# Optimization experiments

Hardware: AMD Instinct MI355X
Metric: run time of the kernel (lower is better)

The kernel has to match this reference:

```python
import jax, jax.numpy as jnp
import numpy as np

FS = 16000
M = 800            # win_length = 0.05*fs
K = 1024           # n_fft = next pow2
HOP = 600          # M - V, V = M//4
NBINS = 256        # 4000*K//fs
L_MAX = 13         # round(0.5*fs/hop)
L_MIN = 3
MIN_DB = 10.0
DEFAULT_RT60 = 0.5
EPS = 1e-10
INVALID = 1e30


def _stft_power(y):
    # y: [B,1,T] -> power spectrogram [B,1,NBINS,nF] (torchaudio Spectrogram, power=2,
    # center=True reflect pad, periodic hann of length M zero-padded centered to K)
    n = jnp.arange(M, dtype=y.dtype)
    win = 0.5 - 0.5 * jnp.cos(2.0 * jnp.pi * n / M)
    w = jnp.zeros(K, dtype=y.dtype).at[(K - M) // 2:(K - M) // 2 + M].set(win)
    yp = jnp.pad(y, ((0, 0), (0, 0), (K // 2, K // 2)), mode='reflect')
    nF = 1 + (yp.shape[-1] - K) // HOP
    idx = jnp.arange(nF)[:, None] * HOP + jnp.arange(K)[None, :]
    frames = yp[..., idx] * w                       # [B,1,nF,K]
    spec = jnp.abs(jnp.fft.rfft(frames)) ** 2       # [B,1,nF,K//2+1]
    return jnp.swapaxes(spec, -1, -2)[..., :NBINS, :]


def reference(y, coeffs):
    Y = _stft_power(y)                              # [B,1,F,T]
    B = Y.shape[0]
    T = Y.shape[-1]
    Yf = Y.reshape(B, -1, T)                        # [B,F,T] (mono channel folded)

    # --- strictly-decreasing run detection for every window length L in [3,13] ---
    d = (jnp.diff(Yf, axis=-1) < 0).astype(jnp.int32)                      # [B,F,T-1]
    c = jnp.concatenate([jnp.zeros_like(d[..., :1]), jnp.cumsum(d, -1)], -1)  # [B,F,T]
    Ls = jnp.arange(L_MIN, L_MAX + 1)               # [11]
    t = jnp.arange(T)
    end = jnp.minimum(t[None, :] + Ls[:, None] - 1, T - 1)                 # [11,T]
    cnt = jnp.take(c, end, axis=-1) - c[:, :, None, :]                     # [B,F,11,T]
    valid_t = (t[None, :] + Ls[:, None]) <= T                              # [11,T]
    dec = (cnt == (Ls - 1)[None, None, :, None]) & valid_t[None, None]     # [B,F,11,T]

    # per subband: largest L with any decreasing window (compute_individual_masks)
    hasL = dec.any(-1)                              # [B,F,11]
    chosen = (Ls.shape[0] - 1) - jnp.argmax(hasL[..., ::-1], -1)           # [B,F]
    has_any = hasL.any(-1)                          # [B,F]
    start_mask = jnp.take_along_axis(dec, chosen[..., None, None], axis=2)[:, :, 0, :]
    start_mask = start_mask & has_any[..., None]    # [B,F,T]
    lenL = L_MIN + chosen                           # [B,F] window length per subband

    # --- padded windows of length L_MAX for every start position ---
    widx = jnp.clip(t[:, None] + jnp.arange(L_MAX)[None, :], 0, T - 1)     # [T,13]
    W = jnp.take(Yf, widx, axis=-1)                 # [B,F,T,13]
    lm = (jnp.arange(L_MAX) < lenL[..., None])[:, :, None, :]              # [B,F,1,13]
    lmf = lm.astype(W.dtype)

    # EDC = reversed cumsum of power, in dB, rescaled to start at 0
    wm = W * lmf
    edc = jnp.cumsum(wm[..., ::-1], -1)[..., ::-1]
    edc_db = 10.0 * jnp.log10(jnp.maximum(edc, EPS))
    scaled = edc_db - edc_db[..., :1]               # [B,F,T,13]

    last_idx = jnp.broadcast_to((lenL - 1)[:, :, None, None], scaled.shape[:-1] + (1,))
    last = jnp.take_along_axis(scaled, last_idx, -1)[..., 0]               # [B,F,T]
    selected = last < -MIN_DB

    x = jnp.arange(L_MAX, dtype=scaled.dtype)
    nl = lenL.astype(scaled.dtype)[..., None]       # [B,F,1]
    xm = jnp.sum(x * lmf[:, :, 0, :], -1, keepdims=True) / nl              # [B,F,1]
    ym = jnp.sum(scaled * lmf, -1) / nl             # [B,F,T]
    xc = (x - xm[..., None]) * lmf                  # [B,F,1,13]
    num = jnp.sum(xc * (scaled - ym[..., None]), -1)                        # [B,F,T]
    den = jnp.sum(xc * xc, -1)                      # [B,F,1]
    slope = num / den

    valid = start_mask & selected
    slope_safe = jnp.where(valid, slope, -1.0)
    rt60 = (-60.0 / slope_safe) * (HOP / FS)        # [B,F,T]

    # per-batch lower median over all valid segments (torch.median semantics)
    vals = jnp.where(valid, rt60, INVALID).reshape(B, -1)
    nvalid = valid.reshape(B, -1).sum(-1)
    srt = jnp.sort(vals, -1)
    midx = jnp.maximum((nvalid - 1) // 2, 0)
    med = jnp.take_along_axis(srt, midx[:, None], -1)[:, 0]
    med = jnp.where(nvalid > 0, med, 0.0)

    corr = coeffs[0] + coeffs[1] * med              # degree-1 polynomial correction
    out = jnp.where(nvalid > 0, corr, DEFAULT_RT60)
    out = jnp.maximum(out, 0.01)
    return out[:, None, None]                       # [B,1,1]


def setup_inputs() -> dict:
    key = jax.random.key(0)
    k1, _ = jax.random.split(key)
    y = jax.random.normal(k1, (32, 1, 160000), dtype=jnp.float32)
    coeffs = jnp.array([0.0, 1.0], dtype=jnp.float32)  # identity polynomial init
    return {"y": y, "coeffs": coeffs}
```

## Files before the change

### kernel.cpp

```cpp
#include <hip/hip_runtime.h>
#include <hip/hip_bf16.h>
#include <math.h>

#define NB 32
#define TLEN 160000
#define HOP 600
#define NBINS 256
#define TT 267
#define TTP 268
#define NROWS (NB * NBINS)
#define LMAX 13

__device__ __forceinline__ unsigned f2key(float f) {
    unsigned b = __float_as_uint(f);
    return (b & 0x80000000u) ? ~b : (b | 0x80000000u);
}
__device__ __forceinline__ int P(int i) { return i + (i >> 4); }
__device__ __forceinline__ int Q(int i) { return i ^ ((i >> 4) & 0x3C); }
__device__ __forceinline__ float2 cmul(float2 a, float2 w) {
    return make_float2(a.x * w.x - a.y * w.y, a.x * w.y + a.y * w.x);
}
__device__ __forceinline__ float2 cadd(float2 a, float2 b) { return make_float2(a.x + b.x, a.y + b.y); }
__device__ __forceinline__ float2 csub(float2 a, float2 b) { return make_float2(a.x - b.x, a.y - b.y); }

__global__ void init_kernel(float2* __restrict__ tw, float* __restrict__ wtab) {
    int j = blockIdx.x * blockDim.x + threadIdx.x;
    if (j < 512) {
        double ang = -2.0 * 3.14159265358979323846 * (double)j / 1024.0;
        tw[j] = make_float2((float)cos(ang), (float)sin(ang));
    }
    if (j < 800) {
        float arg = (6.2831855f * (float)j) / 800.0f;
        wtab[j] = 0.5f - 0.5f * cosf(arg);
    }
}

__global__ __launch_bounds__(256) void stft_power_kernel(
        const float* __restrict__ y, const float2* __restrict__ twg,
        const float* __restrict__ wtab, float* __restrict__ Y) {
    __shared__ float2 zz[4][1024];
    __shared__ float2 twl[544];

    const int g = blockIdx.x;
    const int b = blockIdx.y;
    const int tid = threadIdx.x;
    const int f0 = 8 * g;

    for (int j = tid; j < 512; j += 256) twl[P(j)] = twg[j];

    const float* yb = y + (size_t)b * TLEN;
    #pragma unroll
    for (int a = 0; a < 4; ++a) {
        const int fa = f0 + 2 * a;
        if (fa >= TT) break;
        const bool hasB = (fa + 1 < TT);
        const int base = fa * HOP - 512;
        const int i = 4 * tid;
        float2 q4[4];
        if (base >= 0 && hasB) {
            if (i >= 112 && i < 912) {
                float4 w4 = *(const float4*)(wtab + (i - 112));
                float4 a0 = *(const float4*)(yb + base + i);
                float4 a1 = *(const float4*)(yb + base + HOP + i);
                q4[0] = make_float2(a0.x * w4.x, a1.x * w4.x);
                q4[1] = make_float2(a0.y * w4.y, a1.y * w4.y);
                q4[2] = make_float2(a0.z * w4.z, a1.z * w4.z);
                q4[3] = make_float2(a0.w * w4.w, a1.w * w4.w);
            } else {
                q4[0] = q4[1] = q4[2] = q4[3] = make_float2(0.f, 0.f);
            }
        } else {
            #pragma unroll
            for (int m = 0; m < 4; ++m) {
                const int ii = i + m;
                float v0 = 0.f, v1 = 0.f;
                if (ii >= 112 && ii < 912) {
                    float w = wtab[ii - 112];
                    int p0 = base + ii;
                    int q0 = p0 < 0 ? -p0 : p0;
                    v0 = yb[q0] * w;
                    if (hasB) v1 = yb[p0 + HOP] * w;
                }
                q4[m] = make_float2(v0, v1);
            }
        }
        float4* dst = (float4*)&zz[a][Q(i)];
        dst[0] = make_float4(q4[0].x, q4[0].y, q4[1].x, q4[1].y);
        dst[1] = make_float4(q4[2].x, q4[2].y, q4[3].x, q4[3].y);
    }
    __syncthreads();

    {
        const int a = tid >> 6, j = tid & 63;
        float2 x[16];
        #pragma unroll
        for (int k = 0; k < 16; ++k) x[k] = zz[a][Q(j + 64 * k)];
        #pragma unroll
        for (int k = 0; k < 8; ++k) {
            float2 s = csub(x[k], x[k + 8]);
            x[k] = cadd(x[k], x[k + 8]);
            x[k + 8] = cmul(s, twl[P(j + 64 * k)]);
        }
        #pragma unroll
        for (int h = 0; h < 16; h += 8)
            #pragma unroll
            for (int k = 0; k < 4; ++k) {
                float2 s = csub(x[h + k], x[h + k + 4]);
                x[h + k] = cadd(x[h + k], x[h + k + 4]);
                x[h + k + 4] = cmul(s, twl[P(2 * j + 128 * k)]);
            }
        #pragma unroll
        for (int h = 0; h < 16; h += 4)
            #pragma unroll
            for (int k = 0; k < 2; ++k) {
                float2 s = csub(x[h + k], x[h + k + 2]);
                x[h + k] = cadd(x[h + k], x[h + k + 2]);
                x[h + k + 2] = cmul(s, twl[P(4 * j + 256 * k)]);
            }
        {
            const float2 wD = twl[P(8 * j)];
            #pragma unroll
            for (int h = 0; h < 16; h += 2) {
                float2 s = csub(x[h], x[h + 1]);
                x[h] = cadd(x[h], x[h + 1]);
                x[h + 1] = cmul(s, wD);
            }
        }
        #pragma unroll
        for (int k = 0; k < 16; ++k) zz[a][Q(j + 64 * k)] = x[k];
    }
    __syncthreads();

    {
        const int a = tid >> 6, l = tid & 63;
        const int gg = l >> 2, j2 = l & 3;
        const int b0 = 64 * gg + j2;
        float2 x[16];
        #pragma unroll
        for (int k = 0; k < 16; ++k) x[k] = zz[a][Q(b0 + 4 * k)];
        #pragma unroll
        for (int k = 0; k < 8; ++k) {
            float2 s = csub(x[k], x[k + 8]);
            x[k] = cadd(x[k], x[k + 8]);
            x[k + 8] = cmul(s, twl[P(16 * j2 + 64 * k)]);
        }
        #pragma unroll
        for (int h = 0; h < 16; h += 8)
            #pragma unroll
            for (int k = 0; k < 4; ++k) {
                float2 s = csub(x[h + k], x[h + k + 4]);
                x[h + k] = cadd(x[h + k], x[h + k + 4]);
                x[h + k + 4] = cmul(s, twl[P(32 * j2 + 128 * k)]);
            }
        #pragma unroll
        for (int h = 0; h < 16; h += 4)
            #pragma unroll
            for (int k = 0; k < 2; ++k) {
                float2 s = csub(x[h + k], x[h + k + 2]);
                x[h + k] = cadd(x[h + k], x[h + k + 2]);
                x[h + k + 2] = cmul(s, twl[P(64 * (j2 + 4 * k))]);
            }
        {
            const float2 wD = twl[P(128 * j2)];
            #pragma unroll
            for (int h = 0; h < 16; h += 2) {
                float2 s = csub(x[h], x[h + 1]);
                x[h] = cadd(x[h], x[h + 1]);
                x[h + 1] = cmul(s, wD);
            }
        }
        #pragma unroll
        for (int k = 0; k < 16; ++k) zz[a][Q(b0 + 4 * k)] = x[k];
    }
    __syncthreads();

    #pragma unroll
    for (int a = 0; a < 4; ++a) {
        float4* pp = (float4*)&zz[a][Q(4 * tid)];
        float4 r0 = pp[0], r1 = pp[1];
        float2 x0 = make_float2(r0.x, r0.y), x1 = make_float2(r0.z, r0.w);
        float2 x2 = make_float2(r1.x, r1.y), x3 = make_float2(r1.z, r1.w);
        float2 e0 = cadd(x0, x2);
        float2 e1 = cadd(x1, x3);
        float2 d0 = csub(x0, x2);
        float2 d1 = csub(x1, x3);
        float2 d1m = make_float2(d1.y, -d1.x);
        pp[0] = make_float4(e0.x + e1.x, e0.y + e1.y, e0.x - e1.x, e0.y - e1.y);
        pp[1] = make_float4(d0.x + d1m.x, d0.y + d1m.y, d0.x - d1m.x, d0.y - d1m.y);
    }
    __syncthreads();

    const int k = tid;
    const int nk = (1024 - k) & 1023;
    const int rk = (int)(__brev((unsigned)k) >> 22);
    const int rn = (int)(__brev((unsigned)nk) >> 22);
    float* yrow = Y + ((size_t)b * NBINS + k) * TTP;
    if (g < 33) {
        float p[8];
        #pragma unroll
        for (int a = 0; a < 4; ++a) {
            float2 zk = zz[a][Q(rk)], zn = zz[a][Q(rn)];
            float x0r = 0.5f * (zk.x + zn.x), x0i = 0.5f * (zk.y - zn.y);
            float x1r = 0.5f * (zk.y + zn.y), x1i = 0.5f * (zn.x - zk.x);
            p[2 * a]     = x0r * x0r + x0i * x0i;
            p[2 * a + 1] = x1r * x1r + x1i * x1i;
        }
        *(float4*)(yrow + f0)     = make_float4(p[0], p[1], p[2], p[3]);
        *(float4*)(yrow + f0 + 4) = make_float4(p[4], p[5], p[6], p[7]);
    } else {
        #pragma unroll
        for (int a = 0; a < 4; ++a) {
            const int fb2 = f0 + 2 * a;
            if (fb2 >= TT) break;
            float2 zk = zz[a][Q(rk)], zn = zz[a][Q(rn)];
            float x0r = 0.5f * (zk.x + zn.x), x0i = 0.5f * (zk.y - zn.y);
            float x1r = 0.5f * (zk.y + zn.y), x1i = 0.5f * (zn.x - zk.x);
            if (fb2 + 1 < TT)
                *(float2*)(yrow + fb2) = make_float2(x0r * x0r + x0i * x0i,
                                                     x1r * x1r + x1i * x1i);
            else
                yrow[fb2] = x0r * x0r + x0i * x0i;
        }
    }
}

__global__ __launch_bounds__(256) void subband_kernel(
        const float* __restrict__ Y, unsigned* __restrict__ compact,
        int* __restrict__ rowcnt) {
    __shared__ float ys[4][272];

    const int tid = threadIdx.x;
    const int lane = tid & 63;
    const int wave = tid >> 6;
    const int row = blockIdx.x * 4 + wave;
    const float* src = Y + (size_t)row * TTP;

    float v[5];
    #pragma unroll
    for (int c = 0; c < 5; ++c) {
        int t = c * 64 + lane;
        v[c] = (t < TT) ? src[t] : 0.0f;
        if (t < TT) ys[wave][t] = v[c];
    }
    __syncthreads();

    const float* yy = ys[wave];

    unsigned long long m[5];
    #pragma unroll
    for (int c = 0; c < 5; ++c) {
        int t = c * 64 + lane;
        bool d = (t < TT - 1) && (yy[t + 1] < v[c]);
        m[c] = __ballot(d);
    }

    auto runl = [&](int c, int l) -> int {
        unsigned long long lo = m[c] >> l;
        if (l && c < 4) lo |= m[c + 1] << (64 - l);
        unsigned win = (unsigned)lo & 0xFFFu;
        return (win == 0xFFFu) ? 12 : (__ffs((int)~win) - 1);
    };

    int rl[5];
    int mx = 0;
    #pragma unroll
    for (int c = 0; c < 5; ++c) { rl[c] = runl(c, lane); mx = max(mx, rl[c]); }
    #pragma unroll
    for (int o = 32; o; o >>= 1) mx = max(mx, __shfl_xor(mx, o));
    const int maxrun = mx;

    if (maxrun < 2) {
        if (lane == 0) rowcnt[row] = 0;
        return;
    }
    const int L = maxrun + 1;

    float sumx = 0.0f;
    #pragma unroll
    for (int j = 0; j < LMAX; ++j) if (j < L) sumx += (float)j;
    const float xm = sumx / (float)L;
    float den = 0.0f;
    #pragma unroll
    for (int j = 0; j < LMAX; ++j) if (j < L) { float xc = (float)j - xm; den += xc * xc; }

    unsigned keys[5];
    unsigned long long vm[5];
    #pragma unroll
    for (int c = 0; c < 5; ++c) {
        const int t = c * 64 + lane;
        bool sel = false;
        unsigned key = 0u;
        if (rl[c] >= L - 1) {
            float edc[LMAX];
            float s = 0.0f;
            #pragma unroll
            for (int j = LMAX - 1; j >= 0; --j) {
                if (j < L) s += yy[t + j];
                edc[j] = s;
            }
            float db0 = 10.0f * log10f(fmaxf(edc[0], 1e-10f));
            float scl[LMAX];
            float s1 = 0.0f;
            float last = 0.0f;
            #pragma unroll
            for (int j = 0; j < LMAX; ++j) {
                if (j < L) {
                    float db = 10.0f * log10f(fmaxf(edc[j], 1e-10f));
                    float sc = db - db0;
                    scl[j] = sc;
                    s1 += sc;
                    if (j == L - 1) last = sc;
                }
            }
            if (last < -10.0f) {
                const float ym = s1 / (float)L;
                float num = 0.0f;
                #pragma unroll
                for (int j = 0; j < LMAX; ++j)
                    if (j < L) num += ((float)j - xm) * (scl[j] - ym);
                const float slope = num / den;
                float rt60 = (-60.0f / slope) * 0.0375f;
                sel = true;
                key = f2key(rt60);
            }
        }
        vm[c] = __ballot(sel);
        keys[c] = key;
    }

    unsigned* dst = compact + (size_t)row * TTP;
    const unsigned long long below = (1ull << lane) - 1ull;
    int base = 0;
    #pragma unroll
    for (int c = 0; c < 5; ++c) {
        if (vm[c] & (1ull << lane))
            dst[base + (int)__popcll(vm[c] & below)] = keys[c];
        base += (int)__popcll(vm[c]);
    }
    if (lane == 0) rowcnt[row] = base;
}

__global__ __launch_bounds__(256) void median_kernel(
        const unsigned* __restrict__ compact, const int* __restrict__ rowcnt,
        const float* __restrict__ coeffs, float* __restrict__ out) {
    __shared__ unsigned hist[16384];
    __shared__ unsigned wsum[4];
    __shared__ int sh_sel;
    __shared__ unsigned sh_kkc;
    __shared__ unsigned sh_kk, sh_prefix, sh_pmask;
    __shared__ int sh_n;

    const int b = blockIdx.x;
    const int tid = threadIdx.x;
    const int lane = tid & 63;
    const int wave = tid >> 6;
    const int myrow = b * NBINS + tid;
    const int myc = rowcnt[myrow];
    const unsigned* mykeys = compact + (size_t)myrow * TTP;

    {
        unsigned x = (unsigned)myc;
        #pragma unroll
        for (int o = 1; o < 64; o <<= 1) { unsigned t = __shfl_up(x, o); if (lane >= o) x += t; }
        if (lane == 63) wsum[wave] = x;
        __syncthreads();
        if (tid == 0) {
            int n = (int)(wsum[0] + wsum[1] + wsum[2] + wsum[3]);
            sh_n = n;
            sh_kk = (n > 0) ? (unsigned)((n - 1) / 2) : 0u;
            sh_prefix = 0u; sh_pmask = 0u;
        }
        __syncthreads();
    }
    const int n = sh_n;
    if (n == 0) {
        if (tid == 0) out[b] = 0.5f;
        return;
    }

    const int shifts[3] = {18, 4, 0};
    for (int p = 0; p < 3; ++p) {
        const int shift = shifts[p];
        const bool big = (p < 2);

        if (big) {
            uint4* h4 = (uint4*)hist;
            for (int i = tid; i < 4096; i += 256) h4[i] = make_uint4(0u, 0u, 0u, 0u);
        } else if (tid < 16) hist[tid] = 0u;
        __syncthreads();

        const unsigned pfx = sh_prefix, pm = sh_pmask;
        const unsigned bmask = big ? 16383u : 15u;
        for (int i = 0; i < myc; ++i) {
            unsigned k = mykeys[i];
            if ((k & pm) == pfx) atomicAdd(&hist[(k >> shift) & bmask], 1u);
        }
        __syncthreads();

        const unsigned kk = sh_kk;
        if (big) {
            unsigned s = 0;
            const int base = tid * 64;
            #pragma unroll 8
            for (int ii = 0; ii < 64; ++ii) s += hist[base + ((ii + tid) & 63)];
            unsigned x = s;
            #pragma unroll
            for (int o = 1; o < 64; o <<= 1) { unsigned t = __shfl_up(x, o); if (lane >= o) x += t; }
            if (lane == 63) wsum[wave] = x;
            __syncthreads();
            unsigned woff = 0;
            for (int w = 0; w < wave; ++w) woff += wsum[w];
            const unsigned incl = x + woff, excl = incl - s;
            if (kk >= excl && kk < incl) { sh_sel = tid; sh_kkc = kk - excl; }
            __syncthreads();
            const int sel = sh_sel;
            const unsigned kkc = sh_kkc;
            if (wave == 0) {
                unsigned h = hist[sel * 64 + lane];
                unsigned xx = h;
                #pragma unroll
                for (int o = 1; o < 64; o <<= 1) { unsigned t = __shfl_up(xx, o); if (lane >= o) xx += t; }
                unsigned ex = xx - h;
                if (kkc >= ex && kkc < xx) {
                    sh_prefix = pfx | ((unsigned)(sel * 64 + lane) << shift);
                    sh_pmask  = pm | (16383u << shift);
                    sh_kk = kkc - ex;
                }
            }
            __syncthreads();
        } else {
            if (wave == 0) {
                unsigned h = (lane < 16) ? hist[lane] : 0u;
                unsigned xx = h;
                #pragma unroll
                for (int o = 1; o < 64; o <<= 1) { unsigned t = __shfl_up(xx, o); if (lane >= o) xx += t; }
                unsigned ex = xx - h;
                if (lane < 16 && kk >= ex && kk < xx)
                    sh_prefix = pfx | (unsigned)lane;
            }
            __syncthreads();
        }
    }

    if (tid == 0) {
        unsigned kx = sh_prefix;
        unsigned fb = (kx & 0x80000000u) ? (kx & 0x7FFFFFFFu) : ~kx;
        float med = __uint_as_float(fb);
        out[b] = fmaxf(coeffs[0] + coeffs[1] * med, 0.01f);
    }
}

extern "C" void kernel_launch(void* const* d_in, const int* in_sizes, int n_in,
                              void* d_out, int out_size, void* d_ws, size_t ws_size,
                              hipStream_t stream) {
    const float* y = (const float*)d_in[0];
    const float* coeffs = (const float*)d_in[1];
    float* out = (float*)d_out;

    const size_t YB = (size_t)NROWS * TTP * sizeof(float);
    char* base = (char*)d_ws;
    float* Y = (float*)base;
    unsigned* compact = (unsigned*)(base + YB);
    int* rowcnt = (int*)(base + 2 * YB);
    float2* tw = (float2*)(base + 2 * YB + (size_t)NROWS * sizeof(int));
    float* wtab = (float*)((char*)tw + 512 * sizeof(float2));

    init_kernel<<<4, 256, 0, stream>>>(tw, wtab);
    stft_power_kernel<<<dim3((TT + 7) / 8, NB), 256, 0, stream>>>(y, tw, wtab, Y);
    subband_kernel<<<NROWS / 4, 256, 0, stream>>>(Y, compact, rowcnt);
    median_kernel<<<NB, 256, 0, stream>>>(compact, rowcnt, coeffs, out);
}
```

Measured before the change: 104.6 us.

## Stage median keys in LDS and use 12/12/8-bit radix select passes

The median kernel now compacts each batch's valid keys into shared memory once, using a prefix-sum offset per row. Each radix pass then scans those keys with all threads striding over them, instead of every thread re-reading its own row from global memory with uneven per-thread counts. The radix digits change from 14/14/4 bits to 12/12/8, which shrinks the histogram to 4096 bins so it is cheaper to clear and scan. This costs extra LDS (64KB of key staging) and keeps a global-memory fallback for when there are more than 16384 keys.

```diff
diff --git a/kernel.cpp b/kernel.cpp
--- a/kernel.cpp
+++ b/kernel.cpp
@@ -343,12 +343,11 @@
 __global__ __launch_bounds__(256) void median_kernel(
         const unsigned* __restrict__ compact, const int* __restrict__ rowcnt,
         const float* __restrict__ coeffs, float* __restrict__ out) {
-    __shared__ unsigned hist[16384];
+    __shared__ unsigned lkeys[16384];
+    __shared__ unsigned hist[4096];
     __shared__ unsigned wsum[4];
-    __shared__ int sh_sel;
-    __shared__ unsigned sh_kkc;
-    __shared__ unsigned sh_kk, sh_prefix, sh_pmask;
-    __shared__ int sh_n;
+    __shared__ unsigned sh_kk, sh_kkc, sh_prefix, sh_pmask;
+    __shared__ int sh_sel, sh_n;
 
     const int b = blockIdx.x;
     const int tid = threadIdx.x;
@@ -358,85 +357,95 @@
     const int myc = rowcnt[myrow];
     const unsigned* mykeys = compact + (size_t)myrow * TTP;
 
-    {
-        unsigned x = (unsigned)myc;
-        #pragma unroll
-        for (int o = 1; o < 64; o <<= 1) { unsigned t = __shfl_up(x, o); if (lane >= o) x += t; }
-        if (lane == 63) wsum[wave] = x;
-        __syncthreads();
-        if (tid == 0) {
-            int n = (int)(wsum[0] + wsum[1] + wsum[2] + wsum[3]);
-            sh_n = n;
-            sh_kk = (n > 0) ? (unsigned)((n - 1) / 2) : 0u;
-            sh_prefix = 0u; sh_pmask = 0u;
-        }
-        __syncthreads();
-    }
+    unsigned x = (unsigned)myc;
+    #pragma unroll
+    for (int o = 1; o < 64; o <<= 1) { unsigned t = __shfl_up(x, o); if (lane >= o) x += t; }
+    if (lane == 63) wsum[wave] = x;
+    __syncthreads();
+    unsigned woff = 0;
+    for (int w = 0; w < wave; ++w) woff += wsum[w];
+    const int myoff = (int)(woff + x) - myc;
+    if (tid == 0) {
+        int n = (int)(wsum[0] + wsum[1] + wsum[2] + wsum[3]);
+        sh_n = n;
+        sh_kk = (n > 0) ? (unsigned)((n - 1) / 2) : 0u;
+        sh_prefix = 0u; sh_pmask = 0u;
+    }
+    __syncthreads();
     const int n = sh_n;
     if (n == 0) {
         if (tid == 0) out[b] = 0.5f;
         return;
     }
 
-    const int shifts[3] = {18, 4, 0};
+    const bool inlds = (n <= 16384);
+    if (inlds)
+        for (int i = 0; i < myc; ++i) lkeys[myoff + i] = mykeys[i];
+    __syncthreads();
+
+    const int shifts[3] = {20, 8, 0};
     for (int p = 0; p < 3; ++p) {
         const int shift = shifts[p];
         const bool big = (p < 2);
-
+        const unsigned bmask = big ? 4095u : 255u;
+
+        {
+            uint4* h4 = (uint4*)hist;
+            for (int i = tid; i < 1024; i += 256) h4[i] = make_uint4(0u, 0u, 0u, 0u);
+        }
+        __syncthreads();
+
+        const unsigned pfx = sh_prefix, pm = sh_pmask;
+        if (inlds) {
+            for (int i = tid; i < n; i += 256) {
+                unsigned k = lkeys[i];
+                if ((k & pm) == pfx) atomicAdd(&hist[(k >> shift) & bmask], 1u);
+            }
+        } else {
+            for (int i = 0; i < myc; ++i) {
+                unsigned k = mykeys[i];
+                if ((k & pm) == pfx) atomicAdd(&hist[(k >> shift) & bmask], 1u);
+            }
+        }
+        __syncthreads();
+
+        const unsigned kk = sh_kk;
+        unsigned s = 0;
         if (big) {
-            uint4* h4 = (uint4*)hist;
-            for (int i = tid; i < 4096; i += 256) h4[i] = make_uint4(0u, 0u, 0u, 0u);
-        } else if (tid < 16) hist[tid] = 0u;
+            const int base2 = tid * 16;
+            #pragma unroll
+            for (int ii = 0; ii < 16; ++ii) s += hist[base2 + ((ii + tid) & 15)];
+        } else {
+            s = hist[tid];
+        }
+        unsigned xs = s;
+        #pragma unroll
+        for (int o = 1; o < 64; o <<= 1) { unsigned t = __shfl_up(xs, o); if (lane >= o) xs += t; }
+        if (lane == 63) wsum[wave] = xs;
         __syncthreads();
-
-        const unsigned pfx = sh_prefix, pm = sh_pmask;
-        const unsigned bmask = big ? 16383u : 15u;
-        for (int i = 0; i < myc; ++i) {
-            unsigned k = mykeys[i];
-            if ((k & pm) == pfx) atomicAdd(&hist[(k >> shift) & bmask], 1u);
+        unsigned wo = 0;
+        for (int w = 0; w < wave; ++w) wo += wsum[w];
+        const unsigned incl = xs + wo, excl = incl - s;
+        if (kk >= excl && kk < incl) {
+            if (big) { sh_sel = tid; sh_kkc = kk - excl; }
+            else     { sh_prefix = pfx | (unsigned)tid; }
         }
         __syncthreads();
 
-        const unsigned kk = sh_kk;
         if (big) {
-            unsigned s = 0;
-            const int base = tid * 64;
-            #pragma unroll 8
-            for (int ii = 0; ii < 64; ++ii) s += hist[base + ((ii + tid) & 63)];
-            unsigned x = s;
-            #pragma unroll
-            for (int o = 1; o < 64; o <<= 1) { unsigned t = __shfl_up(x, o); if (lane >= o) x += t; }
-            if (lane == 63) wsum[wave] = x;
-            __syncthreads();
-            unsigned woff = 0;
-            for (int w = 0; w < wave; ++w) woff += wsum[w];
-            const unsigned incl = x + woff, excl = incl - s;
-            if (kk >= excl && kk < incl) { sh_sel = tid; sh_kkc = kk - excl; }
-            __syncthreads();
             const int sel = sh_sel;
             const unsigned kkc = sh_kkc;
             if (wave == 0) {
-                unsigned h = hist[sel * 64 + lane];
+                unsigned h = (lane < 16) ? hist[sel * 16 + lane] : 0u;
                 unsigned xx = h;
                 #pragma unroll
                 for (int o = 1; o < 64; o <<= 1) { unsigned t = __shfl_up(xx, o); if (lane >= o) xx += t; }
                 unsigned ex = xx - h;
-                if (kkc >= ex && kkc < xx) {
-                    sh_prefix = pfx | ((unsigned)(sel * 64 + lane) << shift);
-                    sh_pmask  = pm | (16383u << shift);
+                if (lane < 16 && kkc >= ex && kkc < xx) {
+                    sh_prefix = pfx | ((unsigned)(sel * 16 + lane) << shift);
+                    sh_pmask  = pm | (bmask << shift);
                     sh_kk = kkc - ex;
                 }
-            }
-            __syncthreads();
-        } else {
-            if (wave == 0) {
-                unsigned h = (lane < 16) ? hist[lane] : 0u;
-                unsigned xx = h;
-                #pragma unroll
-                for (int o = 1; o < 64; o <<= 1) { unsigned t = __shfl_up(xx, o); if (lane >= o) xx += t; }
-                unsigned ex = xx - h;
-                if (lane < 16 && kk >= ex && kk < xx)
-                    sh_prefix = pfx | (unsigned)lane;
             }
             __syncthreads();
         }
```

New measurement: 98.15 us, median of 2. 6.2% less time.
